# Kernel tuning notes

Measured on AMD Instinct MI355X. Metric: run time of the kernel, lower is better.

## Reference

```python
import jax, jax.numpy as jnp
import numpy as np

BSZ, L, P, H = 8, 8192, 128, 128


def setup_inputs() -> dict:
    key = jax.random.key(0)
    ks = jax.random.split(key, 7)
    x = jax.random.normal(ks[0], (BSZ, L, H), jnp.float32)
    A_diag = jax.random.uniform(ks[1], (P,), jnp.float32, 0.0, 2.0)
    G_diag = jax.random.uniform(ks[2], (P,), jnp.float32, 0.0, 1.0)
    dt = jax.random.normal(ks[3], (P,), jnp.float32)
    B = jax.random.uniform(ks[4], (P, H, 2), jnp.float32, -1.0, 1.0) / np.sqrt(H)
    C = jax.random.uniform(ks[5], (H, P, 2), jnp.float32, -1.0, 1.0) / np.sqrt(P)
    D = jax.random.normal(ks[6], (H,), jnp.float32)
    return {"x": x, "A_diag": A_diag, "G_diag": G_diag, "dt": dt, "B": B, "C": C, "D": D}


def _project_G(G, A, dt):
    # clamp G >= 0 and fold A into the valid stability interval [A_low, A_high]
    G = jnp.maximum(G, 0.0)
    dt2 = jnp.maximum(dt ** 2, 1e-06)
    s = jnp.sqrt(1.0 + dt * G)
    A_low = (2.0 + dt * G - 2.0 * s) / dt2
    A_high = (2.0 + dt * G + 2.0 * s) / dt2
    A_proj = A_low + jax.nn.relu(A - A_low) - jax.nn.relu(A - A_high)
    return A_proj, G


def _binop(q_i, q_j):
    # 2x2 block (per diagonal state p) recurrence composition: M_j @ M_i
    A_i, b_i = q_i
    A_j, b_j = q_j
    A_new = jnp.einsum('...ikp,...kjp->...ijp', A_j, A_i)
    b_new = jnp.einsum('...ikp,...kp->...ip', A_j, b_i) + b_j
    return A_new, b_new


def reference(x, A_diag, G_diag, dt, B, C, D):
    # _project_A_dt
    dt_s = jax.nn.sigmoid(dt)                       # (P,)
    A = jnp.maximum(A_diag, 0.0)
    # G_base = projected G given (A, dt)
    _, G_base = _project_G(G_diag, A, dt_s)
    # constant damping: G_seq is G_base broadcast over time, then re-projected per step
    G_seq = jnp.broadcast_to(G_base, (L, P))        # (L,P)
    A_seq, G_seq = _project_G(G_seq, A, dt_s)       # broadcasts over L
    A_fin = jnp.min(A_seq, axis=0)                  # (P,)
    # complex input projection Bu_k = B_complex @ u_k
    Bc = B[..., 0] + 1j * B[..., 1]                 # (P,H)
    Cc = C[..., 0] + 1j * C[..., 1]                 # (H,P)
    Bu = jnp.einsum('blh,ph->blp', x, Bc)           # (BSZ,L,P) complex64
    # IMEX transition coefficients
    S = 1.0 + dt_s * G_seq                          # (L,P)
    M11 = 1.0 / S
    M12 = -(dt_s / S) * A_fin
    M21 = dt_s / S
    M22 = 1.0 - (dt_s ** 2 / S) * A_fin
    M = jnp.stack([jnp.stack([M11, M12], axis=-2),
                   jnp.stack([M21, M22], axis=-2)], axis=-3)   # (L,2,2,P) real
    F = jnp.stack([(dt_s / S) * Bu, (dt_s ** 2 / S) * Bu], axis=-2)  # (BSZ,L,2,P) complex
    M_b = jnp.broadcast_to(M, (BSZ,) + M.shape)     # (BSZ,L,2,2,P)
    _, xs = jax.lax.associative_scan(_binop, (M_b, F), axis=1)
    ys = xs[..., 1, :]                              # (BSZ,L,P) complex: x-component
    out = jnp.einsum('blp,hp->blh', ys, Cc).real + D * x
    return out
```

## Files before the change

### kernel.cpp

```cpp
#include <hip/hip_runtime.h>
#include <math.h>

#define BSZ_ 8
#define LEN_ 8192
#define NC_  128
#define CT_  64

typedef __attribute__((ext_vector_type(8))) short bf16x8;
typedef __attribute__((ext_vector_type(4))) float f32x4;

#define OFF_PRM 0
#define OFF_W1T 2048
#define OFF_W2T (OFF_W1T + 16384)
#define OFF_MPW (OFF_W2T + 16384)
#define OFF_SUM (OFF_MPW + 16640)
#define OFF_V2  (OFF_SUM + BSZ_*NC_*256*2)

__device__ __forceinline__ unsigned short f2bf(float f) {
    unsigned u = __builtin_bit_cast(unsigned, f);
    u += 0x7fffu + ((u >> 16) & 1u);
    return (unsigned short)(u >> 16);
}

__device__ __forceinline__ unsigned short f2bf_fast(float f) {
    unsigned u = __builtin_bit_cast(unsigned, f);
    return (unsigned short)((u + 0x8000u) >> 16);
}

__device__ __forceinline__ float bf2f(unsigned short u) {
    return __builtin_bit_cast(float, (unsigned)u << 16);
}

__global__ __launch_bounds__(256) void k_setup(const float* __restrict__ A_diag,
                                               const float* __restrict__ G_diag,
                                               const float* __restrict__ dt,
                                               const float* __restrict__ B,
                                               const float* __restrict__ C,
                                               float* __restrict__ ws)
{
    int i = blockIdx.x * 256 + threadIdx.x;
    {
        int pc = i >> 7, h = i & 127;
        int p = pc >> 1, cc = pc & 1;
        float dts = 1.f / (1.f + expf(-dt[p]));
        float G = fmaxf(G_diag[p], 0.f);
        float c1 = dts / (1.f + dts * G);
        ((unsigned short*)(ws + OFF_W1T))[i] = f2bf(c1 * B[p * 256 + h * 2 + cc]);
    }
    {
        float v = C[i];
        ((unsigned short*)(ws + OFF_W2T))[i] = f2bf((i & 1) ? -v : v);
    }
    if (i < 8192) {
        int k = (i >> 7) + 1;
        int p = i & 127;
        float dtv = dt[p];
        float dts = 1.f / (1.f + expf(-dtv));
        float A   = fmaxf(A_diag[p], 0.f);
        float G   = fmaxf(G_diag[p], 0.f);
        float dt2 = fmaxf(dts * dts, 1e-6f);
        float s   = sqrtf(1.f + dts * G);
        float A_low  = (2.f + dts * G - 2.f * s) / dt2;
        float A_high = (2.f + dts * G + 2.f * s) / dt2;
        float Af = A_low + fmaxf(A - A_low, 0.f) - fmaxf(A - A_high, 0.f);
        float S   = 1.f + dts * G;
        float M11 = 1.f / S;
        float M12 = -(dts / S) * Af;
        float M21 = dts / S;
        float M22 = 1.f - (dts * dts / S) * Af;

        float r11 = 1.f, r12 = 0.f, r21 = 0.f, r22 = 1.f;
        float b11 = M11, b12 = M12, b21 = M21, b22 = M22;
        int kk = k;
#pragma unroll
        for (int it = 0; it < 7; ++it) {
            if (kk & 1) {
                float t11 = b11 * r11 + b12 * r21;
                float t12 = b11 * r12 + b12 * r22;
                float t21 = b21 * r11 + b22 * r21;
                float t22 = b21 * r12 + b22 * r22;
                r11 = t11; r12 = t12; r21 = t21; r22 = t22;
            }
            float s11 = b11 * b11 + b12 * b21;
            float s12 = b11 * b12 + b12 * b22;
            float s21 = b21 * b11 + b22 * b21;
            float s22 = b21 * b12 + b22 * b22;
            b11 = s11; b12 = s12; b21 = s21; b22 = s22;
            kk >>= 1;
        }
        float2* MPW = (float2*)(ws + OFF_MPW);
        MPW[k * 128 + p] = make_float2(r21, r22);

        float* prm = ws + OFF_PRM + p * 16;
        if (k == 1) {
            prm[0] = M11; prm[1] = M12; prm[2] = M21; prm[3] = M22; prm[4] = dts;
        }
        if (k == 64) {
            prm[5] = r11; prm[6] = r12; prm[7] = r21; prm[8] = r22;
        }
    }
}

__device__ __forceinline__ void stage_x(const float* __restrict__ X, size_t row0,
                                        int tid, unsigned short (*xs)[136])
{
    int r = tid >> 4, cl = (tid & 15) * 8;
#pragma unroll
    for (int i = 0; i < 4; ++i) {
        int rr = r + i * 16;
        const float* src = X + (row0 + rr) * 128 + cl;
        float4 v0 = *(const float4*)src;
        float4 v1 = *(const float4*)(src + 4);
        unsigned short* dst = &xs[rr][cl];
        dst[0] = f2bf_fast(v0.x); dst[1] = f2bf_fast(v0.y); dst[2] = f2bf_fast(v0.z); dst[3] = f2bf_fast(v0.w);
        dst[4] = f2bf_fast(v1.x); dst[5] = f2bf_fast(v1.y); dst[6] = f2bf_fast(v1.z); dst[7] = f2bf_fast(v1.w);
    }
}

__device__ __forceinline__ void gemm1_acc(const unsigned short (*xs)[136],
                                          const unsigned short* __restrict__ W1T,
                                          int wv, int lane, f32x4 acc[4][4])
{
    int l15 = lane & 15, quad = lane >> 4;
    int nbase = wv * 64;
#pragma unroll
    for (int kk = 0; kk < 4; ++kk) {
        int k0 = kk * 32 + quad * 8;
        bf16x8 af[4], bg[4];
#pragma unroll
        for (int mi = 0; mi < 4; ++mi) af[mi] = *(const bf16x8*)&xs[mi * 16 + l15][k0];
#pragma unroll
        for (int nj = 0; nj < 4; ++nj)
            bg[nj] = *(const bf16x8*)(W1T + (size_t)(nbase + nj * 16 + l15) * 128 + k0);
#pragma unroll
        for (int mi = 0; mi < 4; ++mi)
#pragma unroll
            for (int nj = 0; nj < 4; ++nj)
                acc[mi][nj] = __builtin_amdgcn_mfma_f32_16x16x32_bf16(af[mi], bg[nj], acc[mi][nj], 0, 0, 0);
    }
}

__global__ __launch_bounds__(256) void k_fuse1(const float* __restrict__ X,
                                               float* __restrict__ ws)
{
    __shared__ __align__(16) char smem[32 * 260 * 4];
    unsigned short (*xs)[136] = (unsigned short (*)[136])smem;
    float (*fl)[260] = (float (*)[260])smem;

    int tid = threadIdx.x;
    int b = blockIdx.x >> 7, c = blockIdx.x & 127;
    size_t row0 = (size_t)b * LEN_ + (size_t)c * CT_;

    stage_x(X, row0, tid, xs);
    __syncthreads();

    int wv = tid >> 6, lane = tid & 63;
    int l15 = lane & 15, quad = lane >> 4, nbase = wv * 64;
    f32x4 acc[4][4] = {};
    gemm1_acc(xs, (const unsigned short*)(ws + OFF_W1T), wv, lane, acc);
    __syncthreads();

    const float* prm = ws + OFF_PRM + (tid >> 1) * 16;
    float M11 = prm[0], M12 = prm[1], dts = prm[4];
    unsigned short* V2b = (unsigned short*)(ws + OFF_V2);
    float h1 = 0.f, h2 = 0.f;

#pragma unroll
    for (int half = 0; half < 2; ++half) {
#pragma unroll
        for (int mi = 0; mi < 2; ++mi)
#pragma unroll
            for (int nj = 0; nj < 4; ++nj)
#pragma unroll
                for (int r = 0; r < 4; ++r)
                    fl[mi * 16 + quad * 4 + r][nbase + nj * 16 + l15] =
                        acc[half * 2 + mi][nj][r];
        __syncthreads();
#pragma unroll 8
        for (int t = 0; t < 32; ++t) {
            float u = fl[t][tid];
            float n1 = fmaf(M11, h1, fmaf(M12, h2, u));
            float n2 = fmaf(dts, n1, h2);
            h1 = n1; h2 = n2;
            V2b[(row0 + half * 32 + t) * 256 + tid] = f2bf_fast(h2);
        }
        __syncthreads();
    }
    *(float2*)(ws + OFF_SUM + (((size_t)b * NC_ + c) * 256 + tid) * 2) = make_float2(h1, h2);
}

__global__ __launch_bounds__(64) void k_scan2(float* __restrict__ ws)
{
    int b = blockIdx.x >> 2, cg = blockIdx.x & 3;
    int ch = cg * 64 + threadIdx.x;
    const float* prm = ws + OFF_PRM + (ch >> 1) * 16;
    float T11 = prm[5], T12 = prm[6], T21 = prm[7], T22 = prm[8];
    float e1 = 0.f, e2 = 0.f;
    float* base = ws + OFF_SUM + (size_t)b * 65536 + ch * 2;
#pragma unroll 8
    for (int j = 0; j < NC_; ++j) {
        float2 l = *(float2*)(base + (size_t)j * 512);
        *(float2*)(base + (size_t)j * 512) = make_float2(e1, e2);
        float n1 = fmaf(T11, e1, fmaf(T12, e2, l.x));
        float n2 = fmaf(T21, e1, fmaf(T22, e2, l.y));
        e1 = n1; e2 = n2;
    }
}

__global__ __launch_bounds__(256) void k_fuse2(const float* __restrict__ X,
                                               const float* __restrict__ Dv,
                                               float* __restrict__ ws,
                                               float* __restrict__ out)
{
    __shared__ __align__(16) unsigned short ysb[64][264];

    int tid = threadIdx.x;
    int b = blockIdx.x >> 7, c = blockIdx.x & 127;
    size_t row0 = (size_t)b * LEN_ + (size_t)c * CT_;

    {
        int q = tid & 127;
        int tseg = tid >> 7;
        float4 Cp = *(const float4*)(ws + OFF_SUM +
                                     (((size_t)b * NC_ + c) * 256 + 2 * q) * 2);
        const float2* MPW = (const float2*)(ws + OFF_MPW);
        const unsigned short* V2b = (const unsigned short*)(ws + OFF_V2) +
                                    (row0 + tseg * 32) * 256 + 2 * q;
#pragma unroll 8
        for (int t = 0; t < 32; ++t) {
            int tt = tseg * 32 + t;
            ushort2 v2u = *(const ushort2*)(V2b + (size_t)t * 256);
            float2 m = MPW[(tt + 1) * 128 + q];
            float y0 = fmaf(m.x, Cp.x, fmaf(m.y, Cp.y, bf2f(v2u.x)));
            float y1 = fmaf(m.x, Cp.z, fmaf(m.y, Cp.w, bf2f(v2u.y)));
            *(ushort2*)&ysb[tt][2 * q] = make_ushort2(f2bf_fast(y0), f2bf_fast(y1));
        }
    }
    __syncthreads();

    int wv = tid >> 6, lane = tid & 63;
    int l15 = lane & 15, quad = lane >> 4;
    int mrow = (wv & 1) * 32, ncol = (wv >> 1) * 64;
    f32x4 a2[2][4] = {};
    const unsigned short* W2T = (const unsigned short*)(ws + OFF_W2T);
#pragma unroll
    for (int kk = 0; kk < 8; ++kk) {
        int k0 = kk * 32 + quad * 8;
        bf16x8 af[2], bg[4];
#pragma unroll
        for (int mi = 0; mi < 2; ++mi) af[mi] = *(const bf16x8*)&ysb[mrow + mi * 16 + l15][k0];
#pragma unroll
        for (int nj = 0; nj < 4; ++nj)
            bg[nj] = *(const bf16x8*)(W2T + (size_t)(ncol + nj * 16 + l15) * 256 + k0);
#pragma unroll
        for (int mi = 0; mi < 2; ++mi)
#pragma unroll
            for (int nj = 0; nj < 4; ++nj)
                a2[mi][nj] = __builtin_amdgcn_mfma_f32_16x16x32_bf16(af[mi], bg[nj], a2[mi][nj], 0, 0, 0);
    }

#pragma unroll
    for (int mi = 0; mi < 2; ++mi)
#pragma unroll
        for (int nj = 0; nj < 4; ++nj) {
            int col = ncol + nj * 16 + l15;
            float d = Dv[col];
#pragma unroll
            for (int r = 0; r < 4; ++r) {
                size_t gr = row0 + mrow + mi * 16 + quad * 4 + r;
                float xv = X[gr * 128 + col];
                out[gr * 128 + col] = fmaf(d, xv, a2[mi][nj][r]);
            }
        }
}

extern "C" void kernel_launch(void* const* d_in, const int* in_sizes, int n_in,
                              void* d_out, int out_size, void* d_ws, size_t ws_size,
                              hipStream_t stream) {
    const float* x      = (const float*)d_in[0];
    const float* A_diag = (const float*)d_in[1];
    const float* G_diag = (const float*)d_in[2];
    const float* dt     = (const float*)d_in[3];
    const float* B      = (const float*)d_in[4];
    const float* C      = (const float*)d_in[5];
    const float* Dv     = (const float*)d_in[6];
    float* out = (float*)d_out;
    float* ws  = (float*)d_ws;

    k_setup<<<128, 256, 0, stream>>>(A_diag, G_diag, dt, B, C, ws);
    k_fuse1<<<BSZ_ * NC_, 256, 0, stream>>>(x, ws);
    k_scan2<<<32, 64, 0, stream>>>(ws);
    k_fuse2<<<BSZ_ * NC_, 256, 0, stream>>>(x, Dv, ws, out);
}
```

Before: 138.6 us.

## Transpose V2 and power-table layouts and parallelize the chunk-carry scan

```diff
diff --git a/kernel.cpp b/kernel.cpp
--- a/kernel.cpp
+++ b/kernel.cpp
@@ -8,12 +8,14 @@
 
 typedef __attribute__((ext_vector_type(8))) short bf16x8;
 typedef __attribute__((ext_vector_type(4))) float f32x4;
+typedef __attribute__((ext_vector_type(4))) unsigned short u16x4;
+typedef __attribute__((ext_vector_type(8))) unsigned short u16x8;
 
 #define OFF_PRM 0
 #define OFF_W1T 2048
 #define OFF_W2T (OFF_W1T + 16384)
 #define OFF_MPW (OFF_W2T + 16384)
-#define OFF_SUM (OFF_MPW + 16640)
+#define OFF_SUM (OFF_MPW + 16384)
 #define OFF_V2  (OFF_SUM + BSZ_*NC_*256*2)
 
 __device__ __forceinline__ unsigned short f2bf(float f) {
@@ -89,7 +91,7 @@
             kk >>= 1;
         }
         float2* MPW = (float2*)(ws + OFF_MPW);
-        MPW[k * 128 + p] = make_float2(r21, r22);
+        MPW[(size_t)p * 64 + (k - 1)] = make_float2(r21, r22);
 
         float* prm = ws + OFF_PRM + p * 16;
         if (k == 1) {
@@ -97,6 +99,16 @@
         }
         if (k == 64) {
             prm[5] = r11; prm[6] = r12; prm[7] = r21; prm[8] = r22;
+            float u11 = r11, u12 = r12, u21 = r21, u22 = r22;
+#pragma unroll
+            for (int it = 0; it < 4; ++it) {
+                float s11 = u11 * u11 + u12 * u21;
+                float s12 = u11 * u12 + u12 * u22;
+                float s21 = u21 * u11 + u22 * u21;
+                float s22 = u21 * u12 + u22 * u22;
+                u11 = s11; u12 = s12; u21 = s21; u22 = s22;
+            }
+            prm[9] = u11; prm[10] = u12; prm[11] = u21; prm[12] = u22;
         }
     }
 }
@@ -162,7 +174,8 @@
 
     const float* prm = ws + OFF_PRM + (tid >> 1) * 16;
     float M11 = prm[0], M12 = prm[1], dts = prm[4];
-    unsigned short* V2b = (unsigned short*)(ws + OFF_V2);
+    unsigned short* V2T = (unsigned short*)(ws + OFF_V2) +
+                          (((size_t)b * NC_ + c) * 256 + tid) * 64;
     float h1 = 0.f, h2 = 0.f;
 
 #pragma unroll
@@ -176,33 +189,71 @@
                     fl[mi * 16 + quad * 4 + r][nbase + nj * 16 + l15] =
                         acc[half * 2 + mi][nj][r];
         __syncthreads();
-#pragma unroll 8
-        for (int t = 0; t < 32; ++t) {
-            float u = fl[t][tid];
-            float n1 = fmaf(M11, h1, fmaf(M12, h2, u));
-            float n2 = fmaf(dts, n1, h2);
-            h1 = n1; h2 = n2;
-            V2b[(row0 + half * 32 + t) * 256 + tid] = f2bf_fast(h2);
+#pragma unroll
+        for (int g = 0; g < 8; ++g) {
+            u16x4 pk;
+#pragma unroll
+            for (int i = 0; i < 4; ++i) {
+                int t = g * 4 + i;
+                float u = fl[t][tid];
+                float n1 = fmaf(M11, h1, fmaf(M12, h2, u));
+                float n2 = fmaf(dts, n1, h2);
+                h1 = n1; h2 = n2;
+                pk[i] = f2bf_fast(h2);
+            }
+            *(u16x4*)(V2T + half * 32 + g * 4) = pk;
         }
         __syncthreads();
     }
     *(float2*)(ws + OFF_SUM + (((size_t)b * NC_ + c) * 256 + tid) * 2) = make_float2(h1, h2);
 }
 
-__global__ __launch_bounds__(64) void k_scan2(float* __restrict__ ws)
-{
-    int b = blockIdx.x >> 2, cg = blockIdx.x & 3;
-    int ch = cg * 64 + threadIdx.x;
+__global__ __launch_bounds__(256) void k_scan2(float* __restrict__ ws)
+{
+    __shared__ float2 sums[32][8];
+    int blk = blockIdx.x;
+    int b = blk >> 3, chb = (blk & 7) * 32;
+    int tid = threadIdx.x;
+    int chl = tid >> 3, seg = tid & 7;
+    int ch = chb + chl;
     const float* prm = ws + OFF_PRM + (ch >> 1) * 16;
     float T11 = prm[5], T12 = prm[6], T21 = prm[7], T22 = prm[8];
-    float e1 = 0.f, e2 = 0.f;
+    float U11 = prm[9], U12 = prm[10], U21 = prm[11], U22 = prm[12];
     float* base = ws + OFF_SUM + (size_t)b * 65536 + ch * 2;
-#pragma unroll 8
-    for (int j = 0; j < NC_; ++j) {
-        float2 l = *(float2*)(base + (size_t)j * 512);
-        *(float2*)(base + (size_t)j * 512) = make_float2(e1, e2);
-        float n1 = fmaf(T11, e1, fmaf(T12, e2, l.x));
-        float n2 = fmaf(T21, e1, fmaf(T22, e2, l.y));
+
+    float l1[16], l2[16];
+    float s1 = 0.f, s2 = 0.f;
+#pragma unroll
+    for (int j = 0; j < 16; ++j) {
+        float2 l = *(float2*)(base + (size_t)(seg * 16 + j) * 512);
+        l1[j] = l.x; l2[j] = l.y;
+        float n1 = fmaf(T11, s1, fmaf(T12, s2, l.x));
+        float n2 = fmaf(T21, s1, fmaf(T22, s2, l.y));
+        s1 = n1; s2 = n2;
+    }
+    sums[chl][seg] = make_float2(s1, s2);
+    __syncthreads();
+
+    if (seg == 0) {
+        float e1 = 0.f, e2 = 0.f;
+#pragma unroll
+        for (int k = 0; k < 8; ++k) {
+            float2 t = sums[chl][k];
+            sums[chl][k] = make_float2(e1, e2);
+            float n1 = fmaf(U11, e1, fmaf(U12, e2, t.x));
+            float n2 = fmaf(U21, e1, fmaf(U22, e2, t.y));
+            e1 = n1; e2 = n2;
+        }
+    }
+    __syncthreads();
+
+    float2 E = sums[chl][seg];
+    float e1 = E.x, e2 = E.y;
+#pragma unroll
+    for (int j = 0; j < 16; ++j) {
+        *(float2*)(base + (size_t)(seg * 16 + j) * 512) = make_float2(e1, e2);
+        float n1 = fmaf(T11, e1, fmaf(T12, e2, l1[j]));
+        float n2 = fmaf(T21, e1, fmaf(T22, e2, l2[j]));
         e1 = n1; e2 = n2;
     }
 }
@@ -223,17 +274,24 @@
         int tseg = tid >> 7;
         float4 Cp = *(const float4*)(ws + OFF_SUM +
                                      (((size_t)b * NC_ + c) * 256 + 2 * q) * 2);
-        const float2* MPW = (const float2*)(ws + OFF_MPW);
-        const unsigned short* V2b = (const unsigned short*)(ws + OFF_V2) +
-                                    (row0 + tseg * 32) * 256 + 2 * q;
-#pragma unroll 8
-        for (int t = 0; t < 32; ++t) {
-            int tt = tseg * 32 + t;
-            ushort2 v2u = *(const ushort2*)(V2b + (size_t)t * 256);
-            float2 m = MPW[(tt + 1) * 128 + q];
-            float y0 = fmaf(m.x, Cp.x, fmaf(m.y, Cp.y, bf2f(v2u.x)));
-            float y1 = fmaf(m.x, Cp.z, fmaf(m.y, Cp.w, bf2f(v2u.y)));
-            *(ushort2*)&ysb[tt][2 * q] = make_ushort2(f2bf_fast(y0), f2bf_fast(y1));
+        const float2* MP = (const float2*)(ws + OFF_MPW) + (size_t)q * 64;
+        const unsigned short* V2T = (const unsigned short*)(ws + OFF_V2) +
+                                    (((size_t)b * NC_ + c) * 256 + 2 * q) * 64 + tseg * 32;
+#pragma unroll
+        for (int g = 0; g < 4; ++g) {
+            u16x8 va = *(const u16x8*)(V2T + g * 8);
+            u16x8 vb = *(const u16x8*)(V2T + 64 + g * 8);
+#pragma unroll
+            for (int i = 0; i < 4; ++i) {
+                int tt = tseg * 32 + g * 8 + 2 * i;
+                float4 mm = *(const float4*)(MP + tt);
+                float y0 = fmaf(mm.x, Cp.x, fmaf(mm.y, Cp.y, bf2f(va[2 * i])));
+                float y1 = fmaf(mm.x, Cp.z, fmaf(mm.y, Cp.w, bf2f(vb[2 * i])));
+                *(ushort2*)&ysb[tt][2 * q] = make_ushort2(f2bf_fast(y0), f2bf_fast(y1));
+                float y0b = fmaf(mm.z, Cp.x, fmaf(mm.w, Cp.y, bf2f(va[2 * i + 1])));
+                float y1b = fmaf(mm.z, Cp.z, fmaf(mm.w, Cp.w, bf2f(vb[2 * i + 1])));
+                *(ushort2*)&ysb[tt + 1][2 * q] = make_ushort2(f2bf_fast(y0b), f2bf_fast(y1b));
+            }
         }
     }
     __syncthreads();
@@ -289,6 +347,6 @@
 
     k_setup<<<128, 256, 0, stream>>>(A_diag, G_diag, dt, B, C, ws);
     k_fuse1<<<BSZ_ * NC_, 256, 0, stream>>>(x, ws);
-    k_scan2<<<32, 64, 0, stream>>>(ws);
+    k_scan2<<<64, 256, 0, stream>>>(ws);
     k_fuse2<<<BSZ_ * NC_, 256, 0, stream>>>(x, Dv, ws, out);
 }
```

Result: slower. 153.3 us (+10.6%).

## Fuse chunk scan, carry propagation and output GEMM into single decoupled-lookback kernel

Applied to the files above, without the earlier changes.

```diff
diff --git a/kernel.cpp b/kernel.cpp
--- a/kernel.cpp
+++ b/kernel.cpp
@@ -8,13 +8,17 @@
 
 typedef __attribute__((ext_vector_type(8))) short bf16x8;
 typedef __attribute__((ext_vector_type(4))) float f32x4;
+typedef unsigned long long ulong64;
 
 #define OFF_PRM 0
 #define OFF_W1T 2048
 #define OFF_W2T (OFF_W1T + 16384)
 #define OFF_MPW (OFF_W2T + 16384)
-#define OFF_SUM (OFF_MPW + 16640)
-#define OFF_V2  (OFF_SUM + BSZ_*NC_*256*2)
+#define OFF_LOC (OFF_MPW + 16640)
+#define OFF_INC (OFF_LOC + 2 * 1024 * 256)
+#define OFF_CNT (OFF_INC + 2 * 1024 * 256)
+
+#define POISON64 0x7FF0BEEF7FF0BEEFull
 
 __device__ __forceinline__ unsigned short f2bf(float f) {
     unsigned u = __builtin_bit_cast(unsigned, f);
@@ -27,8 +31,13 @@
     return (unsigned short)((u + 0x8000u) >> 16);
 }
 
-__device__ __forceinline__ float bf2f(unsigned short u) {
-    return __builtin_bit_cast(float, (unsigned)u << 16);
+__device__ __forceinline__ void pub8(ulong64* a, float x, float y) {
+    float2 v = make_float2(x, y);
+    __hip_atomic_store(a, __builtin_bit_cast(ulong64, v),
+                       __ATOMIC_RELAXED, __HIP_MEMORY_SCOPE_AGENT);
+}
+__device__ __forceinline__ ulong64 rd8(const ulong64* a) {
+    return __hip_atomic_load((ulong64*)a, __ATOMIC_RELAXED, __HIP_MEMORY_SCOPE_AGENT);
 }
 
 __global__ __launch_bounds__(256) void k_setup(const float* __restrict__ A_diag,
@@ -51,6 +60,13 @@
         float v = C[i];
         ((unsigned short*)(ws + OFF_W2T))[i] = f2bf((i & 1) ? -v : v);
     }
+    {
+        ulong64* L = (ulong64*)(ws + OFF_LOC);
+#pragma unroll
+        for (int k = 0; k < 16; ++k) L[(size_t)k * 32768 + i] = POISON64;
+    }
+    if (i == 0) *(unsigned*)(ws + OFF_CNT) = 0u;
+
     if (i < 8192) {
         int k = (i >> 7) + 1;
         int p = i & 127;
@@ -140,106 +156,118 @@
     }
 }
 
-__global__ __launch_bounds__(256) void k_fuse1(const float* __restrict__ X,
-                                               float* __restrict__ ws)
+__global__ __launch_bounds__(256, 3) void k_main(const float* __restrict__ X,
+                                                 const float* __restrict__ Dv,
+                                                 float* __restrict__ ws,
+                                                 float* __restrict__ out)
 {
-    __shared__ __align__(16) char smem[32 * 260 * 4];
-    unsigned short (*xs)[136] = (unsigned short (*)[136])smem;
-    float (*fl)[260] = (float (*)[260])smem;
+    __shared__ __align__(16) char smem1[17408];
+    __shared__ __align__(16) unsigned short ysb[64][264];
+    __shared__ int vbs;
 
     int tid = threadIdx.x;
-    int b = blockIdx.x >> 7, c = blockIdx.x & 127;
+    if (tid == 0) vbs = (int)atomicAdd((unsigned*)(ws + OFF_CNT), 1u);
+    __syncthreads();
+    int bid = vbs;
+    int b = bid >> 7, c = bid & 127;
     size_t row0 = (size_t)b * LEN_ + (size_t)c * CT_;
 
+    unsigned short (*xs)[136] = (unsigned short (*)[136])smem1;
     stage_x(X, row0, tid, xs);
     __syncthreads();
 
     int wv = tid >> 6, lane = tid & 63;
-    int l15 = lane & 15, quad = lane >> 4, nbase = wv * 64;
+    int l15 = lane & 15, quad = lane >> 4;
     f32x4 acc[4][4] = {};
     gemm1_acc(xs, (const unsigned short*)(ws + OFF_W1T), wv, lane, acc);
-    __syncthreads();
 
     const float* prm = ws + OFF_PRM + (tid >> 1) * 16;
     float M11 = prm[0], M12 = prm[1], dts = prm[4];
-    unsigned short* V2b = (unsigned short*)(ws + OFF_V2);
+    float T11 = prm[5], T12 = prm[6], T21 = prm[7], T22 = prm[8];
+
+    __syncthreads();
+
+    float (*fw)[68] = (float (*)[68])(smem1 + wv * 4352);
+
     float h1 = 0.f, h2 = 0.f;
-
-#pragma unroll
-    for (int half = 0; half < 2; ++half) {
-#pragma unroll
-        for (int mi = 0; mi < 2; ++mi)
-#pragma unroll
-            for (int nj = 0; nj < 4; ++nj)
-#pragma unroll
-                for (int r = 0; r < 4; ++r)
-                    fl[mi * 16 + quad * 4 + r][nbase + nj * 16 + l15] =
-                        acc[half * 2 + mi][nj][r];
-        __syncthreads();
-#pragma unroll 8
-        for (int t = 0; t < 32; ++t) {
-            float u = fl[t][tid];
+#pragma unroll
+    for (int q4 = 0; q4 < 4; ++q4) {
+#pragma unroll
+        for (int nj = 0; nj < 4; ++nj)
+#pragma unroll
+            for (int r = 0; r < 4; ++r)
+                fw[quad * 4 + r][nj * 16 + l15] = acc[q4][nj][r];
+#pragma unroll
+        for (int t = 0; t < 16; ++t) {
+            float u = fw[t][lane];
             float n1 = fmaf(M11, h1, fmaf(M12, h2, u));
             float n2 = fmaf(dts, n1, h2);
             h1 = n1; h2 = n2;
-            V2b[(row0 + half * 32 + t) * 256 + tid] = f2bf_fast(h2);
-        }
-        __syncthreads();
-    }
-    *(float2*)(ws + OFF_SUM + (((size_t)b * NC_ + c) * 256 + tid) * 2) = make_float2(h1, h2);
-}
-
-__global__ __launch_bounds__(64) void k_scan2(float* __restrict__ ws)
-{
-    int b = blockIdx.x >> 2, cg = blockIdx.x & 3;
-    int ch = cg * 64 + threadIdx.x;
-    const float* prm = ws + OFF_PRM + (ch >> 1) * 16;
-    float T11 = prm[5], T12 = prm[6], T21 = prm[7], T22 = prm[8];
-    float e1 = 0.f, e2 = 0.f;
-    float* base = ws + OFF_SUM + (size_t)b * 65536 + ch * 2;
-#pragma unroll 8
-    for (int j = 0; j < NC_; ++j) {
-        float2 l = *(float2*)(base + (size_t)j * 512);
-        *(float2*)(base + (size_t)j * 512) = make_float2(e1, e2);
-        float n1 = fmaf(T11, e1, fmaf(T12, e2, l.x));
-        float n2 = fmaf(T21, e1, fmaf(T22, e2, l.y));
-        e1 = n1; e2 = n2;
-    }
-}
-
-__global__ __launch_bounds__(256) void k_fuse2(const float* __restrict__ X,
-                                               const float* __restrict__ Dv,
-                                               float* __restrict__ ws,
-                                               float* __restrict__ out)
-{
-    __shared__ __align__(16) unsigned short ysb[64][264];
-
-    int tid = threadIdx.x;
-    int b = blockIdx.x >> 7, c = blockIdx.x & 127;
-    size_t row0 = (size_t)b * LEN_ + (size_t)c * CT_;
-
-    {
-        int q = tid & 127;
-        int tseg = tid >> 7;
-        float4 Cp = *(const float4*)(ws + OFF_SUM +
-                                     (((size_t)b * NC_ + c) * 256 + 2 * q) * 2);
-        const float2* MPW = (const float2*)(ws + OFF_MPW);
-        const unsigned short* V2b = (const unsigned short*)(ws + OFF_V2) +
-                                    (row0 + tseg * 32) * 256 + 2 * q;
-#pragma unroll 8
-        for (int t = 0; t < 32; ++t) {
-            int tt = tseg * 32 + t;
-            ushort2 v2u = *(const ushort2*)(V2b + (size_t)t * 256);
-            float2 m = MPW[(tt + 1) * 128 + q];
-            float y0 = fmaf(m.x, Cp.x, fmaf(m.y, Cp.y, bf2f(v2u.x)));
-            float y1 = fmaf(m.x, Cp.z, fmaf(m.y, Cp.w, bf2f(v2u.y)));
-            *(ushort2*)&ysb[tt][2 * q] = make_ushort2(f2bf_fast(y0), f2bf_fast(y1));
+        }
+    }
+
+    ulong64* LOC = (ulong64*)(ws + OFF_LOC);
+    ulong64* INC = (ulong64*)(ws + OFF_INC);
+    size_t me = (size_t)bid * 256 + tid;
+    pub8(&LOC[me], h1, h2);
+
+    float P1 = 0.f, P2 = 0.f;
+    if (c == 0) {
+        pub8(&INC[me], h1, h2);
+    } else {
+        size_t rowb = (size_t)(b * NC_) * 256 + tid;
+        float W11 = 1.f, W12 = 0.f, W21 = 0.f, W22 = 1.f;
+        int j = c - 1;
+        while (true) {
+            ulong64 vi = rd8(&INC[rowb + (size_t)j * 256]);
+            if (vi != POISON64) {
+                float2 I = __builtin_bit_cast(float2, vi);
+                P1 = fmaf(W11, I.x, fmaf(W12, I.y, P1));
+                P2 = fmaf(W21, I.x, fmaf(W22, I.y, P2));
+                break;
+            }
+            ulong64 vl = rd8(&LOC[rowb + (size_t)j * 256]);
+            if (vl != POISON64) {
+                float2 s = __builtin_bit_cast(float2, vl);
+                P1 = fmaf(W11, s.x, fmaf(W12, s.y, P1));
+                P2 = fmaf(W21, s.x, fmaf(W22, s.y, P2));
+                float n11 = W11 * T11 + W12 * T21, n12 = W11 * T12 + W12 * T22;
+                float n21 = W21 * T11 + W22 * T21, n22 = W21 * T12 + W22 * T22;
+                W11 = n11; W12 = n12; W21 = n21; W22 = n22;
+                if (--j < 0) break;
+            } else {
+                __builtin_amdgcn_s_sleep(2);
+            }
+        }
+        float I1 = fmaf(T11, P1, fmaf(T12, P2, h1));
+        float I2 = fmaf(T21, P1, fmaf(T22, P2, h2));
+        pub8(&INC[me], I1, I2);
+    }
+
+    const float2* MPW = (const float2*)(ws + OFF_MPW);
+    int p = tid >> 1;
+    h1 = 0.f; h2 = 0.f;
+#pragma unroll
+    for (int q4 = 0; q4 < 4; ++q4) {
+#pragma unroll
+        for (int nj = 0; nj < 4; ++nj)
+#pragma unroll
+            for (int r = 0; r < 4; ++r)
+                fw[quad * 4 + r][nj * 16 + l15] = acc[q4][nj][r];
+#pragma unroll
+        for (int t = 0; t < 16; ++t) {
+            int tt = q4 * 16 + t;
+            float u = fw[t][lane];
+            float n1 = fmaf(M11, h1, fmaf(M12, h2, u));
+            float n2 = fmaf(dts, n1, h2);
+            h1 = n1; h2 = n2;
+            float2 m = MPW[(tt + 1) * 128 + p];
+            float y = fmaf(m.x, P1, fmaf(m.y, P2, n2));
+            ysb[tt][tid] = f2bf_fast(y);
         }
     }
     __syncthreads();
 
-    int wv = tid >> 6, lane = tid & 63;
-    int l15 = lane & 15, quad = lane >> 4;
     int mrow = (wv & 1) * 32, ncol = (wv >> 1) * 64;
     f32x4 a2[2][4] = {};
     const unsigned short* W2T = (const unsigned short*)(ws + OFF_W2T);
@@ -288,7 +316,5 @@
     float* ws  = (float*)d_ws;
 
     k_setup<<<128, 256, 0, stream>>>(A_diag, G_diag, dt, B, C, ws);
-    k_fuse1<<<BSZ_ * NC_, 256, 0, stream>>>(x, ws);
-    k_scan2<<<32, 64, 0, stream>>>(ws);
-    k_fuse2<<<BSZ_ * NC_, 256, 0, stream>>>(x, Dv, ws, out);
-}
+    k_main<<<BSZ_ * NC_, 256, 0, stream>>>(x, Dv, ws, out);
+}
```

Result: slower. 156.5 us (+12.9%).

## Replace serial chunk-carry scan kernel with direct weighted sum in fuse2

Applied to the files above, without the earlier changes.

```diff
diff --git a/kernel.cpp b/kernel.cpp
--- a/kernel.cpp
+++ b/kernel.cpp
@@ -13,8 +13,9 @@
 #define OFF_W1T 2048
 #define OFF_W2T (OFF_W1T + 16384)
 #define OFF_MPW (OFF_W2T + 16384)
-#define OFF_SUM (OFF_MPW + 16640)
-#define OFF_V2  (OFF_SUM + BSZ_*NC_*256*2)
+#define OFF_TK  (OFF_MPW + 16640)
+#define OFF_SUM (OFF_TK + 65536)
+#define OFF_V2  (OFF_SUM + 524288)
 
 __device__ __forceinline__ unsigned short f2bf(float f) {
     unsigned u = __builtin_bit_cast(unsigned, f);
@@ -51,24 +52,26 @@
         float v = C[i];
         ((unsigned short*)(ws + OFF_W2T))[i] = f2bf((i & 1) ? -v : v);
     }
+    if (i >= 16384) return;
+
+    int p = i & 127;
+    float dtv = dt[p];
+    float dts = 1.f / (1.f + expf(-dtv));
+    float A   = fmaxf(A_diag[p], 0.f);
+    float G   = fmaxf(G_diag[p], 0.f);
+    float dt2 = fmaxf(dts * dts, 1e-6f);
+    float s   = sqrtf(1.f + dts * G);
+    float A_low  = (2.f + dts * G - 2.f * s) / dt2;
+    float A_high = (2.f + dts * G + 2.f * s) / dt2;
+    float Af = A_low + fmaxf(A - A_low, 0.f) - fmaxf(A - A_high, 0.f);
+    float S   = 1.f + dts * G;
+    float M11 = 1.f / S;
+    float M12 = -(dts / S) * Af;
+    float M21 = dts / S;
+    float M22 = 1.f - (dts * dts / S) * Af;
+
     if (i < 8192) {
         int k = (i >> 7) + 1;
-        int p = i & 127;
-        float dtv = dt[p];
-        float dts = 1.f / (1.f + expf(-dtv));
-        float A   = fmaxf(A_diag[p], 0.f);
-        float G   = fmaxf(G_diag[p], 0.f);
-        float dt2 = fmaxf(dts * dts, 1e-6f);
-        float s   = sqrtf(1.f + dts * G);
-        float A_low  = (2.f + dts * G - 2.f * s) / dt2;
-        float A_high = (2.f + dts * G + 2.f * s) / dt2;
-        float Af = A_low + fmaxf(A - A_low, 0.f) - fmaxf(A - A_high, 0.f);
-        float S   = 1.f + dts * G;
-        float M11 = 1.f / S;
-        float M12 = -(dts / S) * Af;
-        float M21 = dts / S;
-        float M22 = 1.f - (dts * dts / S) * Af;
-
         float r11 = 1.f, r12 = 0.f, r21 = 0.f, r22 = 1.f;
         float b11 = M11, b12 = M12, b21 = M21, b22 = M22;
         int kk = k;
@@ -88,16 +91,43 @@
             b11 = s11; b12 = s12; b21 = s21; b22 = s22;
             kk >>= 1;
         }
-        float2* MPW = (float2*)(ws + OFF_MPW);
-        MPW[k * 128 + p] = make_float2(r21, r22);
-
-        float* prm = ws + OFF_PRM + p * 16;
+        ((float2*)(ws + OFF_MPW))[k * 128 + p] = make_float2(r21, r22);
         if (k == 1) {
+            float* prm = ws + OFF_PRM + p * 16;
             prm[0] = M11; prm[1] = M12; prm[2] = M21; prm[3] = M22; prm[4] = dts;
         }
-        if (k == 64) {
-            prm[5] = r11; prm[6] = r12; prm[7] = r21; prm[8] = r22;
-        }
+    }
+
+    {
+        int k = i >> 7;
+        float t11 = M11, t12 = M12, t21 = M21, t22 = M22;
+#pragma unroll
+        for (int it = 0; it < 6; ++it) {
+            float s11 = t11 * t11 + t12 * t21;
+            float s12 = t11 * t12 + t12 * t22;
+            float s21 = t21 * t11 + t22 * t21;
+            float s22 = t21 * t12 + t22 * t22;
+            t11 = s11; t12 = s12; t21 = s21; t22 = s22;
+        }
+        float r11 = 1.f, r12 = 0.f, r21 = 0.f, r22 = 1.f;
+        int kk = k;
+#pragma unroll
+        for (int it = 0; it < 7; ++it) {
+            if (kk & 1) {
+                float n11 = t11 * r11 + t12 * r21;
+                float n12 = t11 * r12 + t12 * r22;
+                float n21 = t21 * r11 + t22 * r21;
+                float n22 = t21 * r12 + t22 * r22;
+                r11 = n11; r12 = n12; r21 = n21; r22 = n22;
+            }
+            float s11 = t11 * t11 + t12 * t21;
+            float s12 = t11 * t12 + t12 * t22;
+            float s21 = t21 * t11 + t22 * t21;
+            float s22 = t21 * t12 + t22 * t22;
+            t11 = s11; t12 = s12; t21 = s21; t22 = s22;
+            kk >>= 1;
+        }
+        ((float4*)(ws + OFF_TK))[k * 128 + p] = make_float4(r11, r12, r21, r22);
     }
 }
 
@@ -189,40 +219,36 @@
     *(float2*)(ws + OFF_SUM + (((size_t)b * NC_ + c) * 256 + tid) * 2) = make_float2(h1, h2);
 }
 
-__global__ __launch_bounds__(64) void k_scan2(float* __restrict__ ws)
-{
-    int b = blockIdx.x >> 2, cg = blockIdx.x & 3;
-    int ch = cg * 64 + threadIdx.x;
-    const float* prm = ws + OFF_PRM + (ch >> 1) * 16;
-    float T11 = prm[5], T12 = prm[6], T21 = prm[7], T22 = prm[8];
-    float e1 = 0.f, e2 = 0.f;
-    float* base = ws + OFF_SUM + (size_t)b * 65536 + ch * 2;
-#pragma unroll 8
-    for (int j = 0; j < NC_; ++j) {
-        float2 l = *(float2*)(base + (size_t)j * 512);
-        *(float2*)(base + (size_t)j * 512) = make_float2(e1, e2);
-        float n1 = fmaf(T11, e1, fmaf(T12, e2, l.x));
-        float n2 = fmaf(T21, e1, fmaf(T22, e2, l.y));
-        e1 = n1; e2 = n2;
-    }
-}
-
 __global__ __launch_bounds__(256) void k_fuse2(const float* __restrict__ X,
                                                const float* __restrict__ Dv,
                                                float* __restrict__ ws,
                                                float* __restrict__ out)
 {
     __shared__ __align__(16) unsigned short ysb[64][264];
+    __shared__ float2 pf[256];
 
     int tid = threadIdx.x;
     int b = blockIdx.x >> 7, c = blockIdx.x & 127;
     size_t row0 = (size_t)b * LEN_ + (size_t)c * CT_;
 
     {
+        float P1 = 0.f, P2 = 0.f;
+        const float2* SUMb = (const float2*)(ws + OFF_SUM) + (size_t)b * NC_ * 256 + tid;
+        const float4* TK = (const float4*)(ws + OFF_TK) + (tid >> 1);
+        for (int j = 0; j < c; ++j) {
+            float2 s = SUMb[(size_t)j * 256];
+            float4 t = TK[(size_t)(c - 1 - j) * 128];
+            P1 = fmaf(t.x, s.x, fmaf(t.y, s.y, P1));
+            P2 = fmaf(t.z, s.x, fmaf(t.w, s.y, P2));
+        }
+        pf[tid] = make_float2(P1, P2);
+    }
+    __syncthreads();
+
+    {
         int q = tid & 127;
         int tseg = tid >> 7;
-        float4 Cp = *(const float4*)(ws + OFF_SUM +
-                                     (((size_t)b * NC_ + c) * 256 + 2 * q) * 2);
+        float2 Ca = pf[2 * q], Cb = pf[2 * q + 1];
         const float2* MPW = (const float2*)(ws + OFF_MPW);
         const unsigned short* V2b = (const unsigned short*)(ws + OFF_V2) +
                                     (row0 + tseg * 32) * 256 + 2 * q;
@@ -231,8 +257,8 @@
             int tt = tseg * 32 + t;
             ushort2 v2u = *(const ushort2*)(V2b + (size_t)t * 256);
             float2 m = MPW[(tt + 1) * 128 + q];
-            float y0 = fmaf(m.x, Cp.x, fmaf(m.y, Cp.y, bf2f(v2u.x)));
-            float y1 = fmaf(m.x, Cp.z, fmaf(m.y, Cp.w, bf2f(v2u.y)));
+            float y0 = fmaf(m.x, Ca.x, fmaf(m.y, Ca.y, bf2f(v2u.x)));
+            float y1 = fmaf(m.x, Cb.x, fmaf(m.y, Cb.y, bf2f(v2u.y)));
             *(ushort2*)&ysb[tt][2 * q] = make_ushort2(f2bf_fast(y0), f2bf_fast(y1));
         }
     }
@@ -289,6 +315,5 @@
 
     k_setup<<<128, 256, 0, stream>>>(A_diag, G_diag, dt, B, C, ws);
     k_fuse1<<<BSZ_ * NC_, 256, 0, stream>>>(x, ws);
-    k_scan2<<<32, 64, 0, stream>>>(ws);
     k_fuse2<<<BSZ_ * NC_, 256, 0, stream>>>(x, Dv, ws, out);
 }
```

New measurement: 167.9 us. 1.21x slower.
